# Kernel optimization log

Hardware: AMD Instinct MI355X
Metric: run time of the kernel (lower is better)

Reference implementation:

```python
import jax, jax.numpy as jnp
import numpy as np

B, L, E, H, D = 2, 2048, 2048, 16, 128
EPS = 1e-6


def _rms(x, scale):
    # RMSNorm over head_dim, computed in float32 (matches torch RMSNorm)
    x32 = x.astype(jnp.float32)
    n = jnp.mean(x32 * x32, axis=-1, keepdims=True)
    return (scale.astype(jnp.float32) * (x32 * jax.lax.rsqrt(n + EPS))).astype(x.dtype)


def _rotary(x, rope):
    # x: [B, L, H, D]; rope: [B, L, D//2, 2]
    xs = x.astype(jnp.float32).reshape(*x.shape[:-1], -1, 2)  # [B,L,H,D/2,2]
    rc = rope.reshape(xs.shape[0], xs.shape[1], 1, xs.shape[3], 2).astype(jnp.float32)
    out = jnp.stack(
        [xs[..., 0] * rc[..., 0] - xs[..., 1] * rc[..., 1],
         xs[..., 1] * rc[..., 0] + xs[..., 0] * rc[..., 1]], -1)
    return out.reshape(x.shape).astype(x.dtype)


def setup_inputs() -> dict:
    key = jax.random.key(0)
    ks = jax.random.split(key, 9)
    s = 0.02  # weight init scale (~kaiming fan_in for E=2048)
    return {
        "inputs_q": jax.random.normal(ks[0], (B, L, E), jnp.float32),
        "inputs_kv": jax.random.normal(ks[1], (B, L, E), jnp.float32),
        "bias": jax.random.normal(ks[2], (B, 1, L, L), jnp.float32),
        "rope_q": jax.random.normal(ks[3], (B, L, D // 2, 2), jnp.float32),
        "rope_k": jax.random.normal(ks[4], (B, L, D // 2, 2), jnp.float32),
        "Wq": jax.random.normal(ks[5], (E, E), jnp.float32) * s,
        "Wk": jax.random.normal(ks[6], (E, E), jnp.float32) * s,
        "Wv": jax.random.normal(ks[7], (E, E), jnp.float32) * s,
        "Wo": jax.random.normal(ks[8], (E, E), jnp.float32) * s,
        "q_scale": jnp.ones((D,), jnp.float32),
        "k_scale": jnp.ones((D,), jnp.float32),
    }


def reference(inputs_q, inputs_kv, bias, rope_q, rope_k, Wq, Wk, Wv, Wo, q_scale, k_scale):
    Bq, Lq, _ = inputs_q.shape
    Lk = inputs_kv.shape[1]
    dtype = inputs_q.dtype
    # QKV projections (torch Linear: y = x @ W.T)
    q = (inputs_q @ Wq.T).reshape(Bq, Lq, H, D)
    k = (inputs_kv @ Wk.T).reshape(Bq, Lk, H, D)
    v = (inputs_kv @ Wv.T).reshape(Bq, Lk, H, D)
    # qk_norm
    q = _rms(q, q_scale)
    k = _rms(k, k_scale)
    # rotary embeddings
    q = _rotary(q, rope_q)
    k = _rotary(k, rope_k)
    # float32_logits
    q = q.astype(jnp.float32)
    k = k.astype(jnp.float32)
    # faithful to torch source: query.div_(depth ** (-0.5)) == q * sqrt(D)
    q = q / (D ** (-0.5))
    logits = jnp.einsum('bqhd,bkhd->bhqk', q, k) + bias.astype(jnp.float32)
    probs = jax.nn.softmax(logits, axis=-1).astype(dtype)
    # dropout_rate = 0.0 -> identity
    x = jnp.einsum('bhqk,bkhd->bqhd', probs, v).reshape(Bq, Lq, E)
    return x @ Wo.T
```

## Files before the change

kernel.cpp:

```cpp
#include <hip/hip_runtime.h>

#define Bb 2
#define Ll 2048
#define Ee 2048
#define Hh 16
#define Dd 128
#define BL (Bb * Ll)
#define LOSCALE 1024.0f
#define INV_LOSCALE (1.0f / 1024.0f)

typedef float f32x4 __attribute__((ext_vector_type(4)));
typedef _Float16 f16x8 __attribute__((ext_vector_type(8)));

__device__ __forceinline__ void gld_lds16(const void* g, void* l) {
  __builtin_amdgcn_global_load_lds((const __attribute__((address_space(1))) void*)g,
                                   (__attribute__((address_space(3))) void*)l, 16, 0, 0);
}

__global__ __launch_bounds__(256) void cvt_f32_f16(const float* __restrict__ in,
                                                   _Float16* __restrict__ out, int n4) {
  int i = blockIdx.x * 256 + threadIdx.x;
  if (i < n4) {
    float4 f = ((const float4*)in)[i];
    _Float16 o[4] = {(_Float16)f.x, (_Float16)f.y, (_Float16)f.z, (_Float16)f.w};
    ((uint2*)out)[i] = *(uint2*)o;
  }
}

__global__ __launch_bounds__(256) void cvt_split(const float* __restrict__ in,
                                                 _Float16* __restrict__ hi,
                                                 _Float16* __restrict__ lo, int n4) {
  int i = blockIdx.x * 256 + threadIdx.x;
  if (i < n4) {
    float4 f = ((const float4*)in)[i];
    float fa[4] = {f.x, f.y, f.z, f.w};
    _Float16 h[4], l[4];
    for (int j = 0; j < 4; ++j) {
      h[j] = (_Float16)fa[j];
      l[j] = (_Float16)((fa[j] - (float)h[j]) * LOSCALE);
    }
    ((uint2*)hi)[i] = *(uint2*)h;
    ((uint2*)lo)[i] = *(uint2*)l;
  }
}

template <typename OutT>
__global__ __launch_bounds__(256, 2) void gemm_bt(const _Float16* __restrict__ A,
                                                  const _Float16* __restrict__ Bw,
                                                  OutT* __restrict__ C, int M, int N, int K) {
  __shared__ _Float16 As[128 * 64];
  __shared__ _Float16 Bs[128 * 64];
  const int tid = threadIdx.x;
  const int wave = tid >> 6, lane = tid & 63;
  const int quad = lane >> 4, l16 = lane & 15;
  const int lrow = lane >> 3, lch = lane & 7;
  const int scol = (lch ^ lrow) * 8;
  const int bm = blockIdx.y * 128, bn = blockIdx.x * 128;
  const int wm = (wave >> 1) * 64, wn = (wave & 1) * 64;

  f32x4 acc[4][4] = {};

  for (int k0 = 0; k0 < K; k0 += 64) {
    for (int i = 0; i < 4; ++i) {
      int br = wave * 32 + i * 8;
      gld_lds16(&A[(size_t)(bm + br + lrow) * K + k0 + scol], &As[br * 64]);
      gld_lds16(&Bw[(size_t)(bn + br + lrow) * K + k0 + scol], &Bs[br * 64]);
    }
    __syncthreads();
    for (int ks = 0; ks < 2; ++ks) {
      f16x8 af[4], bf[4];
      for (int mt = 0; mt < 4; ++mt)
        af[mt] = *(const f16x8*)&As[(wm + mt * 16 + l16) * 64 +
                                    (((ks * 4 + quad) ^ (l16 & 7)) * 8)];
      for (int nt = 0; nt < 4; ++nt)
        bf[nt] = *(const f16x8*)&Bs[(wn + nt * 16 + l16) * 64 +
                                    (((ks * 4 + quad) ^ (l16 & 7)) * 8)];
      for (int mt = 0; mt < 4; ++mt)
        for (int nt = 0; nt < 4; ++nt)
          acc[mt][nt] = __builtin_amdgcn_mfma_f32_16x16x32_f16(af[mt], bf[nt], acc[mt][nt], 0, 0, 0);
    }
    __syncthreads();
  }

  for (int mt = 0; mt < 4; ++mt)
    for (int nt = 0; nt < 4; ++nt)
      for (int r = 0; r < 4; ++r) {
        int m = bm + wm + mt * 16 + quad * 4 + r;
        int n = bn + wn + nt * 16 + l16;
        C[(size_t)m * N + n] = (OutT)acc[mt][nt][r];
      }
}

__global__ __launch_bounds__(256, 2) void gemm_bt_split(
    const _Float16* __restrict__ Ah, const _Float16* __restrict__ Al,
    const _Float16* __restrict__ Bh, const _Float16* __restrict__ Bl,
    float* __restrict__ C, int M, int N, int K) {
  __shared__ _Float16 Ash[128 * 64];
  __shared__ _Float16 Asl[128 * 64];
  __shared__ _Float16 Bsh[128 * 64];
  __shared__ _Float16 Bsl[128 * 64];
  const int tid = threadIdx.x;
  const int wave = tid >> 6, lane = tid & 63;
  const int quad = lane >> 4, l16 = lane & 15;
  const int lrow = lane >> 3, lch = lane & 7;
  const int scol = (lch ^ lrow) * 8;
  const int bm = blockIdx.y * 128, bn = blockIdx.x * 128;
  const int wm = (wave >> 1) * 64, wn = (wave & 1) * 64;

  f32x4 acc_hh[4][4] = {};
  f32x4 acc_cr[4][4] = {};

  for (int k0 = 0; k0 < K; k0 += 64) {
    for (int i = 0; i < 4; ++i) {
      int br = wave * 32 + i * 8;
      size_t ga = (size_t)(bm + br + lrow) * K + k0 + scol;
      size_t gb = (size_t)(bn + br + lrow) * K + k0 + scol;
      gld_lds16(&Ah[ga], &Ash[br * 64]);
      gld_lds16(&Al[ga], &Asl[br * 64]);
      gld_lds16(&Bh[gb], &Bsh[br * 64]);
      gld_lds16(&Bl[gb], &Bsl[br * 64]);
    }
    __syncthreads();
    for (int ks = 0; ks < 2; ++ks) {
      const int sw = ((ks * 4 + quad) ^ (l16 & 7)) * 8;
      f16x8 afh[4], afl[4], bfh[4], bfl[4];
      for (int mt = 0; mt < 4; ++mt) {
        afh[mt] = *(const f16x8*)&Ash[(wm + mt * 16 + l16) * 64 + sw];
        afl[mt] = *(const f16x8*)&Asl[(wm + mt * 16 + l16) * 64 + sw];
      }
      for (int nt = 0; nt < 4; ++nt) {
        bfh[nt] = *(const f16x8*)&Bsh[(wn + nt * 16 + l16) * 64 + sw];
        bfl[nt] = *(const f16x8*)&Bsl[(wn + nt * 16 + l16) * 64 + sw];
      }
      for (int mt = 0; mt < 4; ++mt)
        for (int nt = 0; nt < 4; ++nt) {
          acc_hh[mt][nt] = __builtin_amdgcn_mfma_f32_16x16x32_f16(afh[mt], bfh[nt], acc_hh[mt][nt], 0, 0, 0);
          acc_cr[mt][nt] = __builtin_amdgcn_mfma_f32_16x16x32_f16(afh[mt], bfl[nt], acc_cr[mt][nt], 0, 0, 0);
          acc_cr[mt][nt] = __builtin_amdgcn_mfma_f32_16x16x32_f16(afl[mt], bfh[nt], acc_cr[mt][nt], 0, 0, 0);
        }
    }
    __syncthreads();
  }

  for (int mt = 0; mt < 4; ++mt)
    for (int nt = 0; nt < 4; ++nt)
      for (int r = 0; r < 4; ++r) {
        int m = bm + wm + mt * 16 + quad * 4 + r;
        int n = bn + wn + nt * 16 + l16;
        C[(size_t)m * N + n] = acc_hh[mt][nt][r] + acc_cr[mt][nt][r] * INV_LOSCALE;
      }
}

__global__ __launch_bounds__(256) void transpose_v(const _Float16* __restrict__ V,
                                                   _Float16* __restrict__ Vt) {
  __shared__ _Float16 T[64][72];
  const int bl0 = blockIdx.x * 64, n0 = blockIdx.y * 64;
  const int tid = threadIdx.x;
  for (int c = 0; c < 2; ++c) {
    int chunk = tid + c * 256;
    int r = chunk >> 3, cc = (chunk & 7) * 8;
    *(uint4*)&T[r][cc] = *(const uint4*)&V[(size_t)(bl0 + r) * Ee + n0 + cc];
  }
  __syncthreads();
  const int b = bl0 >> 11;
  const int k0 = bl0 & (Ll - 1);
  for (int c = 0; c < 2; ++c) {
    int chunk = tid + c * 256;
    int nr = chunk >> 3, kc = (chunk & 7) * 8;
    _Float16 tmp[8];
    for (int j = 0; j < 8; ++j) tmp[j] = T[kc + j][nr];
    *(uint4*)&Vt[((size_t)b * Ee + n0 + nr) * Ll + k0 + kc] = *(uint4*)tmp;
  }
}

__global__ __launch_bounds__(256) void rmsrope(const float* __restrict__ raw,
                                               const float* __restrict__ scale,
                                               const float* __restrict__ rope,
                                               _Float16* __restrict__ outh,
                                               _Float16* __restrict__ outl, float outmul) {
  int row = blockIdx.x * 4 + (threadIdx.x >> 6);
  int t = threadIdx.x & 63;
  float2 x = *(const float2*)&raw[(size_t)row * Dd + 2 * t];
  float ss = x.x * x.x + x.y * x.y;
  for (int off = 1; off < 64; off <<= 1) ss += __shfl_xor(ss, off);
  float inv = rsqrtf(ss * (1.0f / Dd) + 1e-6f);
  float2 sc = *(const float2*)&scale[2 * t];
  float y0 = x.x * inv * sc.x;
  float y1 = x.y * inv * sc.y;
  int bl = row >> 4;
  float2 cs = *(const float2*)&rope[(size_t)bl * Dd + 2 * t];
  float r0 = (y0 * cs.x - y1 * cs.y) * outmul;
  float r1 = (y1 * cs.x + y0 * cs.y) * outmul;
  _Float16 h[2] = {(_Float16)r0, (_Float16)r1};
  _Float16 l[2] = {(_Float16)((r0 - (float)h[0]) * LOSCALE),
                   (_Float16)((r1 - (float)h[1]) * LOSCALE)};
  *(uint*)&outh[(size_t)row * Dd + 2 * t] = *(uint*)h;
  *(uint*)&outl[(size_t)row * Dd + 2 * t] = *(uint*)l;
}

__global__ __launch_bounds__(512, 4) void attn(const _Float16* __restrict__ Qh_,
                                               const _Float16* __restrict__ Ql_,
                                               const _Float16* __restrict__ Kh_,
                                               const _Float16* __restrict__ Kl_,
                                               const _Float16* __restrict__ Vt_g,
                                               const _Float16* __restrict__ bias16,
                                               _Float16* __restrict__ O) {
  __shared__ _Float16 Ksh[64 * 128];
  __shared__ _Float16 Ksl[64 * 128];
  __shared__ _Float16 Vts[128 * 64];
  __shared__ _Float16 Ps[128 * 72];

  const int tid = threadIdx.x;
  const int wave = tid >> 6, lane = tid & 63;
  const int quad = lane >> 4, l16 = lane & 15;
  const int lrow8 = lane >> 3, lch8 = lane & 7;
  const int lrow16 = lane >> 4, lch16 = lane & 15;
  const int h = blockIdx.x;
  const int q0 = blockIdx.y * 128;
  const int b = blockIdx.z;

  f16x8 aqh[4], aql[4];
  {
    size_t qrow = (((size_t)b * Ll + q0 + wave * 16 + l16) * Hh + h) * Dd;
    for (int ks = 0; ks < 4; ++ks) {
      aqh[ks] = *(const f16x8*)&Qh_[qrow + ks * 32 + quad * 8];
      aql[ks] = *(const f16x8*)&Ql_[qrow + ks * 32 + quad * 8];
    }
  }
  const _Float16* Vbase = Vt_g + ((size_t)b * Ee + h * Dd) * Ll;
  const _Float16* biasb = bias16 + (size_t)b * Ll * Ll;

  f32x4 o_acc[8] = {};
  float m_r[4], l_r[4];
  for (int r = 0; r < 4; ++r) { m_r[r] = -1e30f; l_r[r] = 0.f; }

  for (int kt = 0; kt < Ll / 64; ++kt) {
    const int k0 = kt * 64;
    for (int i = 0; i < 2; ++i) {
      int br = wave * 8 + i * 4;
      int row = br + lrow16;
      int sc = (lch16 ^ (row & 7)) * 8;
      size_t g = (((size_t)b * Ll + k0 + row) * Hh + h) * Dd + sc;
      gld_lds16(&Kh_[g], &Ksh[br * 128]);
      gld_lds16(&Kl_[g], &Ksl[br * 128]);
    }
    for (int i = 0; i < 2; ++i) {
      int br = wave * 16 + i * 8;
      int row = br + lrow8;
      int sc = (lch8 ^ (row & 7)) * 8;
      gld_lds16(&Vbase[(size_t)row * Ll + k0 + sc], &Vts[br * 64]);
    }
    for (int i = 0; i < 2; ++i) {
      int gq = q0 + wave * 16 + i * 8 + lrow8;
      gld_lds16(&biasb[(size_t)gq * Ll + k0 + lch8 * 8], &Ps[wave * 1152 + i * 512]);
    }
    __syncthreads();

    f32x4 s_hh[4] = {}, s_cr[4] = {};
    for (int ks = 0; ks < 4; ++ks) {
      const int sw = ((ks * 4 + quad) ^ (l16 & 7)) * 8;
      for (int nt = 0; nt < 4; ++nt) {
        f16x8 bkh = *(const f16x8*)&Ksh[(nt * 16 + l16) * 128 + sw];
        f16x8 bkl = *(const f16x8*)&Ksl[(nt * 16 + l16) * 128 + sw];
        s_hh[nt] = __builtin_amdgcn_mfma_f32_16x16x32_f16(aqh[ks], bkh, s_hh[nt], 0, 0, 0);
        s_cr[nt] = __builtin_amdgcn_mfma_f32_16x16x32_f16(aqh[ks], bkl, s_cr[nt], 0, 0, 0);
        s_cr[nt] = __builtin_amdgcn_mfma_f32_16x16x32_f16(aql[ks], bkh, s_cr[nt], 0, 0, 0);
      }
    }
    for (int nt = 0; nt < 4; ++nt)
      for (int r = 0; r < 4; ++r)
        s_hh[nt][r] += s_cr[nt][r] * INV_LOSCALE +
                       (float)Ps[wave * 1152 + (quad * 4 + r) * 64 + nt * 16 + l16];

    float alpha[4];
    for (int r = 0; r < 4; ++r) {
      float x = fmaxf(fmaxf(s_hh[0][r], s_hh[1][r]), fmaxf(s_hh[2][r], s_hh[3][r]));
      for (int off = 1; off < 16; off <<= 1) x = fmaxf(x, __shfl_xor(x, off));
      float mn = fmaxf(m_r[r], x);
      alpha[r] = __expf(m_r[r] - mn);
      m_r[r] = mn;
    }
    for (int r = 0; r < 4; ++r) {
      float sum = 0.f;
      for (int nt = 0; nt < 4; ++nt) {
        float p = __expf(s_hh[nt][r] - m_r[r]);
        sum += p;
        Ps[(wave * 16 + quad * 4 + r) * 72 + nt * 16 + l16] = (_Float16)p;
      }
      for (int off = 1; off < 16; off <<= 1) sum += __shfl_xor(sum, off);
      l_r[r] = l_r[r] * alpha[r] + sum;
    }
    for (int ot = 0; ot < 8; ++ot)
      for (int r = 0; r < 4; ++r) o_acc[ot][r] *= alpha[r];

    for (int ks = 0; ks < 2; ++ks) {
      const int sw = ((ks * 4 + quad) ^ (l16 & 7)) * 8;
      f16x8 ap = *(const f16x8*)&Ps[(wave * 16 + l16) * 72 + ks * 32 + quad * 8];
      for (int ot = 0; ot < 8; ++ot) {
        f16x8 bv = *(const f16x8*)&Vts[(ot * 16 + l16) * 64 + sw];
        o_acc[ot] = __builtin_amdgcn_mfma_f32_16x16x32_f16(ap, bv, o_acc[ot], 0, 0, 0);
      }
    }
    __syncthreads();
  }

  for (int ot = 0; ot < 8; ++ot)
    for (int r = 0; r < 4; ++r) {
      int m = q0 + wave * 16 + quad * 4 + r;
      O[(((size_t)b * Ll + m) * Hh + h) * Dd + ot * 16 + l16] =
          (_Float16)(o_acc[ot][r] / l_r[r]);
    }
}

extern "C" void kernel_launch(void* const* d_in, const int* in_sizes, int n_in,
                              void* d_out, int out_size, void* d_ws, size_t ws_size,
                              hipStream_t stream) {
  const float* inputs_q  = (const float*)d_in[0];
  const float* inputs_kv = (const float*)d_in[1];
  const float* bias      = (const float*)d_in[2];
  const float* rope_q    = (const float*)d_in[3];
  const float* rope_k    = (const float*)d_in[4];
  const float* Wq        = (const float*)d_in[5];
  const float* Wk        = (const float*)d_in[6];
  const float* Wv        = (const float*)d_in[7];
  const float* Wo        = (const float*)d_in[8];
  const float* q_scale   = (const float*)d_in[9];
  const float* k_scale   = (const float*)d_in[10];
  float* out = (float*)d_out;

  char* ws = (char*)d_ws;
  size_t o = 0;
  auto alloc = [&](size_t bytes) {
    char* p = ws + o;
    o += (bytes + 255) & ~(size_t)255;
    return p;
  };
  const size_t szX16 = (size_t)BL * Ee * 2;
  const size_t szW16 = (size_t)Ee * Ee * 2;
  _Float16* Xq_hi  = (_Float16*)alloc(szX16);
  _Float16* Xq_lo  = (_Float16*)alloc(szX16);
  _Float16* Xkv_hi = (_Float16*)alloc(szX16);
  _Float16* Xkv_lo = (_Float16*)alloc(szX16);
  _Float16* Wq_hi  = (_Float16*)alloc(szW16);
  _Float16* Wq_lo  = (_Float16*)alloc(szW16);
  _Float16* Wk_hi  = (_Float16*)alloc(szW16);
  _Float16* Wk_lo  = (_Float16*)alloc(szW16);
  _Float16* Wv_hi  = (_Float16*)alloc(szW16);
  _Float16* Wo_hi  = (_Float16*)alloc(szW16);
  float* Qraw = (float*)alloc((size_t)BL * Ee * 4);
  float* Kraw = (float*)alloc((size_t)BL * Ee * 4);
  _Float16* V16 = (_Float16*)alloc(szX16);
  _Float16* Q16h   = Xq_hi;
  _Float16* Q16l   = Xq_lo;
  _Float16* K16h   = Xkv_hi;
  _Float16* K16l   = Xkv_lo;
  _Float16* X16    = (_Float16*)Qraw;
  _Float16* Vt_g   = Wq_hi;
  _Float16* bias16 = (_Float16*)Kraw;

  const int nX4 = BL * Ee / 4;
  const int nW4 = Ee * Ee / 4;
  const int nB4 = Bb * Ll * Ll / 4;
  cvt_split<<<nX4 / 256, 256, 0, stream>>>(inputs_q, Xq_hi, Xq_lo, nX4);
  cvt_split<<<nX4 / 256, 256, 0, stream>>>(inputs_kv, Xkv_hi, Xkv_lo, nX4);
  cvt_split<<<nW4 / 256, 256, 0, stream>>>(Wq, Wq_hi, Wq_lo, nW4);
  cvt_split<<<nW4 / 256, 256, 0, stream>>>(Wk, Wk_hi, Wk_lo, nW4);
  cvt_f32_f16<<<nW4 / 256, 256, 0, stream>>>(Wv, Wv_hi, nW4);
  cvt_f32_f16<<<nW4 / 256, 256, 0, stream>>>(Wo, Wo_hi, nW4);

  dim3 gblk(Ee / 128, BL / 128);
  gemm_bt_split<<<gblk, 256, 0, stream>>>(Xq_hi, Xq_lo, Wq_hi, Wq_lo, Qraw, BL, Ee, Ee);
  gemm_bt_split<<<gblk, 256, 0, stream>>>(Xkv_hi, Xkv_lo, Wk_hi, Wk_lo, Kraw, BL, Ee, Ee);
  gemm_bt<_Float16><<<gblk, 256, 0, stream>>>(Xkv_hi, Wv_hi, V16, BL, Ee, Ee);

  transpose_v<<<dim3(BL / 64, Ee / 64), 256, 0, stream>>>(V16, Vt_g);

  rmsrope<<<BL * Hh / 4, 256, 0, stream>>>(Qraw, q_scale, rope_q, Q16h, Q16l, sqrtf((float)Dd));
  rmsrope<<<BL * Hh / 4, 256, 0, stream>>>(Kraw, k_scale, rope_k, K16h, K16l, 1.0f);

  cvt_f32_f16<<<nB4 / 256, 256, 0, stream>>>(bias, bias16, nB4);

  attn<<<dim3(Hh, Ll / 128, Bb), 512, 0, stream>>>(Q16h, Q16l, K16h, K16l, Vt_g, bias16, X16);

  gemm_bt<float><<<gblk, 256, 0, stream>>>(X16, Wo_hi, out, BL, Ee, Ee);
}
```

Before: 783.1 us.

## Double-buffer K/V tiles in attention and pre-permute bias into register fragment layout

The attention kernel now double-buffers the K-hi, K-lo and V shared-memory tiles, prefetching the next key tile while the current one is computed. This is meant to hide global-to-LDS load latency behind the MFMA work. The fp16 bias conversion is replaced by a permute kernel that writes bias in per-lane MFMA fragment order, so each lane loads its 16 bias values directly from global memory instead of staging them through LDS. Shared memory per block roughly doubles, so the launch bound drops from 4 to 2 blocks, which reduces occupancy. The loop still ends with only one barrier while the next tile is prefetched during compute, which may be a buffer-reuse race.

New measurement: 744.7 us. 1.05x faster.

```diff
diff --git a/kernel.cpp b/kernel.cpp
--- a/kernel.cpp
+++ b/kernel.cpp
@@ -6,6 +6,7 @@
 #define Hh 16
 #define Dd 128
 #define BL (Bb * Ll)
+#define NT (Ll / 64)
 #define LOSCALE 1024.0f
 #define INV_LOSCALE (1.0f / 1024.0f)
 
@@ -41,6 +42,34 @@
     }
     ((uint2*)hi)[i] = *(uint2*)h;
     ((uint2*)lo)[i] = *(uint2*)l;
+  }
+}
+
+__global__ __launch_bounds__(256) void bias_perm(const float* __restrict__ bias,
+                                                 _Float16* __restrict__ out) {
+  __shared__ float T[128][68];
+  const int kt = blockIdx.x, qt = blockIdx.y, b = blockIdx.z;
+  const float* src = bias + ((size_t)b * Ll + qt * 128) * Ll + kt * 64;
+  const int t = threadIdx.x;
+  for (int c = 0; c < 8; ++c) {
+    int idx = c * 256 + t;
+    int r = idx >> 4, col4 = (idx & 15) * 4;
+    float4 v = *(const float4*)&src[(size_t)r * Ll + col4];
+    T[r][col4 + 0] = v.x; T[r][col4 + 1] = v.y;
+    T[r][col4 + 2] = v.z; T[r][col4 + 3] = v.w;
+  }
+  __syncthreads();
+  _Float16* dst = out + (((size_t)(b * 16 + qt) * NT + kt) * 8) * 64 * 16;
+  for (int s = 0; s < 2; ++s) {
+    int slot = t + s * 256;
+    int w = slot >> 6, lane = slot & 63;
+    int quad = lane >> 4, l16 = lane & 15;
+    _Float16 vals[16];
+    for (int nt = 0; nt < 4; ++nt)
+      for (int r = 0; r < 4; ++r)
+        vals[nt * 4 + r] = (_Float16)T[w * 16 + quad * 4 + r][nt * 16 + l16];
+    *(uint4*)&dst[(size_t)slot * 16] = *(uint4*)&vals[0];
+    *(uint4*)&dst[(size_t)slot * 16 + 8] = *(uint4*)&vals[8];
   }
 }
 
@@ -198,16 +227,16 @@
   *(uint*)&outl[(size_t)row * Dd + 2 * t] = *(uint*)l;
 }
 
-__global__ __launch_bounds__(512, 4) void attn(const _Float16* __restrict__ Qh_,
+__global__ __launch_bounds__(512, 2) void attn(const _Float16* __restrict__ Qh_,
                                                const _Float16* __restrict__ Ql_,
                                                const _Float16* __restrict__ Kh_,
                                                const _Float16* __restrict__ Kl_,
                                                const _Float16* __restrict__ Vt_g,
-                                               const _Float16* __restrict__ bias16,
+                                               const _Float16* __restrict__ biasp,
                                                _Float16* __restrict__ O) {
-  __shared__ _Float16 Ksh[64 * 128];
-  __shared__ _Float16 Ksl[64 * 128];
-  __shared__ _Float16 Vts[128 * 64];
+  __shared__ _Float16 Ksh[2][64 * 128];
+  __shared__ _Float16 Ksl[2][64 * 128];
+  __shared__ _Float16 Vts[2][128 * 64];
   __shared__ _Float16 Ps[128 * 72];
 
   const int tid = threadIdx.x;
@@ -216,7 +245,7 @@
   const int lrow8 = lane >> 3, lch8 = lane & 7;
   const int lrow16 = lane >> 4, lch16 = lane & 15;
   const int h = blockIdx.x;
-  const int q0 = blockIdx.y * 128;
+  const int qt = blockIdx.y, q0 = qt * 128;
   const int b = blockIdx.z;
 
   f16x8 aqh[4], aql[4];
@@ -228,49 +257,59 @@
     }
   }
   const _Float16* Vbase = Vt_g + ((size_t)b * Ee + h * Dd) * Ll;
-  const _Float16* biasb = bias16 + (size_t)b * Ll * Ll;
+  const _Float16* bias_w =
+      biasp + (((size_t)(b * 16 + qt) * NT * 8 + wave) * 64 + lane) * 16;
 
   f32x4 o_acc[8] = {};
   float m_r[4], l_r[4];
   for (int r = 0; r < 4; ++r) { m_r[r] = -1e30f; l_r[r] = 0.f; }
 
-  for (int kt = 0; kt < Ll / 64; ++kt) {
+  auto stage = [&](int nb, int kt) {
     const int k0 = kt * 64;
     for (int i = 0; i < 2; ++i) {
       int br = wave * 8 + i * 4;
       int row = br + lrow16;
       int sc = (lch16 ^ (row & 7)) * 8;
       size_t g = (((size_t)b * Ll + k0 + row) * Hh + h) * Dd + sc;
-      gld_lds16(&Kh_[g], &Ksh[br * 128]);
-      gld_lds16(&Kl_[g], &Ksl[br * 128]);
+      gld_lds16(&Kh_[g], &Ksh[nb][br * 128]);
+      gld_lds16(&Kl_[g], &Ksl[nb][br * 128]);
     }
     for (int i = 0; i < 2; ++i) {
       int br = wave * 16 + i * 8;
       int row = br + lrow8;
       int sc = (lch8 ^ (row & 7)) * 8;
-      gld_lds16(&Vbase[(size_t)row * Ll + k0 + sc], &Vts[br * 64]);
-    }
-    for (int i = 0; i < 2; ++i) {
-      int gq = q0 + wave * 16 + i * 8 + lrow8;
-      gld_lds16(&biasb[(size_t)gq * Ll + k0 + lch8 * 8], &Ps[wave * 1152 + i * 512]);
-    }
-    __syncthreads();
+      gld_lds16(&Vbase[(size_t)row * Ll + k0 + sc], &Vts[nb][br * 64]);
+    }
+  };
+
+  stage(0, 0);
+  __syncthreads();
+
+  for (int kt = 0; kt < NT; ++kt) {
+    const int cur = kt & 1;
+    if (kt + 1 < NT) stage(cur ^ 1, kt + 1);
+
+    f16x8 bf0 = *(const f16x8*)&bias_w[(size_t)kt * 8192];
+    f16x8 bf1 = *(const f16x8*)&bias_w[(size_t)kt * 8192 + 8];
 
     f32x4 s_hh[4] = {}, s_cr[4] = {};
     for (int ks = 0; ks < 4; ++ks) {
       const int sw = ((ks * 4 + quad) ^ (l16 & 7)) * 8;
       for (int nt = 0; nt < 4; ++nt) {
-        f16x8 bkh = *(const f16x8*)&Ksh[(nt * 16 + l16) * 128 + sw];
-        f16x8 bkl = *(const f16x8*)&Ksl[(nt * 16 + l16) * 128 + sw];
+        f16x8 bkh = *(const f16x8*)&Ksh[cur][(nt * 16 + l16) * 128 + sw];
+        f16x8 bkl = *(const f16x8*)&Ksl[cur][(nt * 16 + l16) * 128 + sw];
         s_hh[nt] = __builtin_amdgcn_mfma_f32_16x16x32_f16(aqh[ks], bkh, s_hh[nt], 0, 0, 0);
         s_cr[nt] = __builtin_amdgcn_mfma_f32_16x16x32_f16(aqh[ks], bkl, s_cr[nt], 0, 0, 0);
         s_cr[nt] = __builtin_amdgcn_mfma_f32_16x16x32_f16(aql[ks], bkh, s_cr[nt], 0, 0, 0);
       }
     }
+#pragma unroll
     for (int nt = 0; nt < 4; ++nt)
-      for (int r = 0; r < 4; ++r)
-        s_hh[nt][r] += s_cr[nt][r] * INV_LOSCALE +
-                       (float)Ps[wave * 1152 + (quad * 4 + r) * 64 + nt * 16 + l16];
+#pragma unroll
+      for (int r = 0; r < 4; ++r) {
+        float bv = (nt < 2) ? (float)bf0[nt * 4 + r] : (float)bf1[nt * 4 + r - 8];
+        s_hh[nt][r] += s_cr[nt][r] * INV_LOSCALE + bv;
+      }
 
     float alpha[4];
     for (int r = 0; r < 4; ++r) {
@@ -297,7 +336,7 @@
       const int sw = ((ks * 4 + quad) ^ (l16 & 7)) * 8;
       f16x8 ap = *(const f16x8*)&Ps[(wave * 16 + l16) * 72 + ks * 32 + quad * 8];
       for (int ot = 0; ot < 8; ++ot) {
-        f16x8 bv = *(const f16x8*)&Vts[(ot * 16 + l16) * 64 + sw];
+        f16x8 bv = *(const f16x8*)&Vts[cur][(ot * 16 + l16) * 64 + sw];
         o_acc[ot] = __builtin_amdgcn_mfma_f32_16x16x32_f16(ap, bv, o_acc[ot], 0, 0, 0);
       }
     }
@@ -356,11 +395,10 @@
   _Float16* K16l   = Xkv_lo;
   _Float16* X16    = (_Float16*)Qraw;
   _Float16* Vt_g   = Wq_hi;
-  _Float16* bias16 = (_Float16*)Kraw;
+  _Float16* biasp  = (_Float16*)Kraw;
 
   const int nX4 = BL * Ee / 4;
   const int nW4 = Ee * Ee / 4;
-  const int nB4 = Bb * Ll * Ll / 4;
   cvt_split<<<nX4 / 256, 256, 0, stream>>>(inputs_q, Xq_hi, Xq_lo, nX4);
   cvt_split<<<nX4 / 256, 256, 0, stream>>>(inputs_kv, Xkv_hi, Xkv_lo, nX4);
   cvt_split<<<nW4 / 256, 256, 0, stream>>>(Wq, Wq_hi, Wq_lo, nW4);
@@ -378,9 +416,9 @@
   rmsrope<<<BL * Hh / 4, 256, 0, stream>>>(Qraw, q_scale, rope_q, Q16h, Q16l, sqrtf((float)Dd));
   rmsrope<<<BL * Hh / 4, 256, 0, stream>>>(Kraw, k_scale, rope_k, K16h, K16l, 1.0f);
 
-  cvt_f32_f16<<<nB4 / 256, 256, 0, stream>>>(bias, bias16, nB4);
-
-  attn<<<dim3(Hh, Ll / 128, Bb), 512, 0, stream>>>(Q16h, Q16l, K16h, K16l, Vt_g, bias16, X16);
+  bias_perm<<<dim3(NT, Ll / 128, Bb), 256, 0, stream>>>(bias, biasp);
+
+  attn<<<dim3(Hh, Ll / 128, Bb), 512, 0, stream>>>(Q16h, Q16l, K16h, K16l, Vt_g, biasp, X16);
 
   gemm_bt<float><<<gblk, 256, 0, stream>>>(X16, Wo_hi, out, BL, Ee, Ee);
 }
```
